# Optimization experiments

Hardware: AMD Instinct MI355X
Metric: run time of the kernel (lower is better)

## Reference

```python
import jax, jax.numpy as jnp
import numpy as np

KW = 31       # avg_pool kernel
PAD = 15      # padding (count_include_pad=True => divide by KW*KW always)


def _box_avg(x):
    # F.avg_pool2d(x, 31, stride=1, padding=15) with count_include_pad=True
    s = jax.lax.reduce_window(
        x, 0.0, jax.lax.add,
        window_dimensions=(1, 1, KW, KW),
        window_strides=(1, 1, 1, 1),
        padding=((0, 0), (0, 0), (PAD, PAD), (PAD, PAD)))
    return s / (KW * KW)


def setup_inputs() -> dict:
    key = jax.random.key(0)
    k1, k2 = jax.random.split(key)
    B, C, H, W = 64, 1, 512, 512
    pred = jax.random.normal(k1, (B, C, H, W), dtype=jnp.float32)
    mask = jax.random.uniform(k2, (B, C, H, W), dtype=jnp.float32)
    return {"pred": pred, "mask": mask}


def reference(pred, mask):
    weit = 1.0 + 5.0 * jnp.abs(_box_avg(mask) - mask)
    # stable BCE-with-logits, elementwise
    bce = jnp.maximum(pred, 0.0) - pred * mask + jnp.log1p(jnp.exp(-jnp.abs(pred)))
    # NOTE: original passes reduce='none' which PyTorch's legacy handling maps to
    # reduction='mean' -> wbce is a global scalar; the weit normalization cancels.
    wbce = bce.mean()  # scalar, broadcast over [B, C]
    p = jax.nn.sigmoid(pred)
    inter = (p * mask * weit).sum(axis=(2, 3))          # [B, C]
    union = ((p + mask) * weit).sum(axis=(2, 3))        # [B, C]
    wiou = 1.0 - (inter + 1.0) / (union - inter + 1.0)  # [B, C]
    return (wbce + wiou).mean()
```

## Files before the change

kernel.cpp:

```cpp
#include <hip/hip_runtime.h>
#include <math.h>

#define BDIM 64
#define HDIM 512
#define WDIM 512
#define KW   31
#define PAD  15
#define INV_KK (1.0f / 961.0f)
#define TH   64
#define NPIX ((size_t)BDIM * HDIM * WDIM)

#define NACC 129

__global__ void zero_acc_kernel(double* acc) {
    int i = threadIdx.x;
    if (i < NACC) acc[i] = 0.0;
}

template<int CTRL, int RMASK>
__device__ __forceinline__ float dpp_add(float p) {
    int t = __builtin_amdgcn_update_dpp(0, __builtin_bit_cast(int, p),
                                        CTRL, RMASK, 0xf, true);
    return p + __builtin_bit_cast(float, t);
}

__device__ __forceinline__ float wave_iscan(float p) {
    p = dpp_add<0x111, 0xf>(p);
    p = dpp_add<0x112, 0xf>(p);
    p = dpp_add<0x114, 0xf>(p);
    p = dpp_add<0x118, 0xf>(p);
    p = dpp_add<0x142, 0xa>(p);
    p = dpp_add<0x143, 0xc>(p);
    return p;
}

__device__ __forceinline__ float wave_iscan30(float p) {
    p = dpp_add<0x111, 0xf>(p);
    p = dpp_add<0x112, 0xf>(p);
    p = dpp_add<0x114, 0xf>(p);
    p = dpp_add<0x118, 0xf>(p);
    p = dpp_add<0x142, 0xa>(p);
    return p;
}

__device__ __forceinline__ float wave_shr1(float p) {
    int t = __builtin_amdgcn_update_dpp(0, __builtin_bit_cast(int, p),
                                        0x138 , 0xf, 0xf, true);
    return __builtin_bit_cast(float, t);
}

__global__ __launch_bounds__(512, 2)
void fused_kernel(const float* __restrict__ pred,
                  const float* __restrict__ mask,
                  double* __restrict__ acc) {
    __shared__ float ring[32][WDIM];
    __shared__ float red[3][8];

    const int b    = blockIdx.x;
    const int y0   = blockIdx.y * TH;
    const int x    = threadIdx.x;
    const int lane = x & 63;
    const int wv   = x >> 6;
    const int s    = wv * 64;

    const float* mbase = mask + (size_t)b * HDIM * WDIM;
    const float* pbase = pred + (size_t)b * HDIM * WDIM;

    const int acol = s - 15 + lane;
    const int bcol = s + 49 + lane;
    const bool a_ok = (acol >= 0) && (acol < WDIM);
    const bool b_ok = (lane < 30) && (bcol < WDIM);

    const int tstart = y0 - PAD;
    const int tend   = y0 + TH - 1 + PAD;

    float vs = 0.f;
    float bce_acc = 0.f, inter_acc = 0.f, uni_acc = 0.f;

    auto load_halo = [&](int row, float& A, float& B) {
        A = 0.f; B = 0.f;
        if (row >= 0 && row < HDIM) {
            const float* rp = mbase + (size_t)row * WDIM;
            if (a_ok) A = rp[acol];
            if (b_ok) B = rp[bcol];
        }
    };
    auto load_emit = [&](int row, float& M, float& P) {
        M = 0.f; P = 0.f;
        if (row >= y0 + PAD && row <= tend) {
            const size_t off = (size_t)(row - PAD) * WDIM + x;
            M = mbase[off];
            P = pbase[off];
        }
    };

    auto process = [&](int t, float A, float B, float M, float P) {
        float pa = wave_iscan(A);
        float pb = wave_iscan30(B);
        const float atot = __builtin_bit_cast(float,
            __builtin_amdgcn_readlane(__builtin_bit_cast(int, pa), 63));
        const float v1 = __shfl(pa, (lane + 30) & 63);
        const float v2 = __shfl(pb, (lane + 30) & 63);
        const float Phi = (lane <= 33) ? v1 : (atot + v2);
        const float Plo = wave_shr1(pa);
        const float hs  = Phi - Plo;

        vs += hs;
        if (t - KW >= tstart) vs -= ring[(t - KW) & 31][x];
        ring[t & 31][x] = hs;

        if (t >= y0 + PAD) {
            const float box  = vs * INV_KK;
            const float weit = 1.f + 5.f * fabsf(box - M);
            const float e1   = __expf(-fabsf(P));
            const float bce  = fmaxf(P, 0.f) - P * M + __logf(1.f + e1);
            const float sp   = __builtin_amdgcn_rcpf(1.f + __expf(-P));
            bce_acc   += bce;
            inter_acc += sp * M * weit;
            uni_acc   += (sp + M) * weit;
        }
    };

    float ca[2], cb[2], cm[2], cp[2];
    load_halo(tstart,     ca[0], cb[0]);
    load_halo(tstart + 1, ca[1], cb[1]);
    load_emit(tstart,     cm[0], cp[0]);
    load_emit(tstart + 1, cm[1], cp[1]);

    for (int t = tstart; t <= tend; t += 2) {
        float na[2], nb[2], nm[2], nq[2];
        load_halo(t + 2, na[0], nb[0]);
        load_halo(t + 3, na[1], nb[1]);
        load_emit(t + 2, nm[0], nq[0]);
        load_emit(t + 3, nm[1], nq[1]);

        process(t,     ca[0], cb[0], cm[0], cp[0]);
        process(t + 1, ca[1], cb[1], cm[1], cp[1]);

        ca[0] = na[0]; ca[1] = na[1]; cb[0] = nb[0]; cb[1] = nb[1];
        cm[0] = nm[0]; cm[1] = nm[1]; cp[0] = nq[0]; cp[1] = nq[1];
    }

#pragma unroll
    for (int off = 32; off > 0; off >>= 1) {
        bce_acc   += __shfl_down(bce_acc, off);
        inter_acc += __shfl_down(inter_acc, off);
        uni_acc   += __shfl_down(uni_acc, off);
    }
    if (lane == 0) {
        red[0][wv] = bce_acc;
        red[1][wv] = inter_acc;
        red[2][wv] = uni_acc;
    }
    __syncthreads();
    if (threadIdx.x == 0) {
        float bs = 0.f, is = 0.f, us = 0.f;
#pragma unroll
        for (int w = 0; w < 8; ++w) { bs += red[0][w]; is += red[1][w]; us += red[2][w]; }
        atomicAdd(&acc[0],      (double)bs);
        atomicAdd(&acc[1 + b],  (double)is);
        atomicAdd(&acc[65 + b], (double)us);
    }
}

__global__ void finalize_kernel(const double* __restrict__ acc, float* __restrict__ out) {
    const int b = threadIdx.x;
    double inter = acc[1 + b];
    double uni   = acc[65 + b];
    double wiou  = 1.0 - (inter + 1.0) / (uni - inter + 1.0);
#pragma unroll
    for (int off = 32; off > 0; off >>= 1) wiou += __shfl_down(wiou, off);
    if (b == 0) {
        double wbce = acc[0] / (double)NPIX;
        out[0] = (float)(wbce + wiou / (double)BDIM);
    }
}

extern "C" void kernel_launch(void* const* d_in, const int* in_sizes, int n_in,
                              void* d_out, int out_size, void* d_ws, size_t ws_size,
                              hipStream_t stream) {
    const float* pred = (const float*)d_in[0];
    const float* mask = (const float*)d_in[1];
    float* out = (float*)d_out;
    double* acc = (double*)d_ws;

    zero_acc_kernel<<<1, 256, 0, stream>>>(acc);

    dim3 grid(BDIM, HDIM / TH);
    fused_kernel<<<grid, WDIM, 0, stream>>>(pred, mask, acc);

    finalize_kernel<<<1, 64, 0, stream>>>(acc, out);
}
```

Before: 175.9 us.

## Move vertical sliding-window ring from LDS to registers and split blocks by width

```diff
diff --git a/kernel.cpp b/kernel.cpp
--- a/kernel.cpp
+++ b/kernel.cpp
@@ -49,19 +49,18 @@
     return __builtin_bit_cast(float, t);
 }
 
-__global__ __launch_bounds__(512, 2)
+__global__ __launch_bounds__(256, 5)
 void fused_kernel(const float* __restrict__ pred,
                   const float* __restrict__ mask,
                   double* __restrict__ acc) {
-    __shared__ float ring[32][WDIM];
-    __shared__ float red[3][8];
+    __shared__ float red[3][4];
 
     const int b    = blockIdx.x;
     const int y0   = blockIdx.y * TH;
-    const int x    = threadIdx.x;
-    const int lane = x & 63;
-    const int wv   = x >> 6;
-    const int s    = wv * 64;
+    const int x    = blockIdx.z * 256 + threadIdx.x;
+    const int lane = threadIdx.x & 63;
+    const int wv   = threadIdx.x >> 6;
+    const int s    = blockIdx.z * 256 + wv * 64;
 
     const float* mbase = mask + (size_t)b * HDIM * WDIM;
     const float* pbase = pred + (size_t)b * HDIM * WDIM;
@@ -70,75 +69,74 @@
     const int bcol = s + 49 + lane;
     const bool a_ok = (acol >= 0) && (acol < WDIM);
     const bool b_ok = (lane < 30) && (bcol < WDIM);
+    const int hi_lane = (lane + 30) & 63;
 
     const int tstart = y0 - PAD;
-    const int tend   = y0 + TH - 1 + PAD;
 
-    float vs = 0.f;
     float bce_acc = 0.f, inter_acc = 0.f, uni_acc = 0.f;
 
-    auto load_halo = [&](int row, float& A, float& B) {
-        A = 0.f; B = 0.f;
-        if (row >= 0 && row < HDIM) {
-            const float* rp = mbase + (size_t)row * WDIM;
+    auto hrow = [&](int t) -> float {
+        float A = 0.f, B = 0.f;
+        if ((unsigned)t < (unsigned)HDIM) {
+            const float* rp = mbase + (size_t)t * WDIM;
             if (a_ok) A = rp[acol];
             if (b_ok) B = rp[bcol];
         }
-    };
-    auto load_emit = [&](int row, float& M, float& P) {
-        M = 0.f; P = 0.f;
-        if (row >= y0 + PAD && row <= tend) {
-            const size_t off = (size_t)(row - PAD) * WDIM + x;
-            M = mbase[off];
-            P = pbase[off];
-        }
-    };
-
-    auto process = [&](int t, float A, float B, float M, float P) {
         float pa = wave_iscan(A);
         float pb = wave_iscan30(B);
         const float atot = __builtin_bit_cast(float,
             __builtin_amdgcn_readlane(__builtin_bit_cast(int, pa), 63));
-        const float v1 = __shfl(pa, (lane + 30) & 63);
-        const float v2 = __shfl(pb, (lane + 30) & 63);
+        const float v1 = __shfl(pa, hi_lane);
+        const float v2 = __shfl(pb, hi_lane);
         const float Phi = (lane <= 33) ? v1 : (atot + v2);
         const float Plo = wave_shr1(pa);
-        const float hs  = Phi - Plo;
-
-        vs += hs;
-        if (t - KW >= tstart) vs -= ring[(t - KW) & 31][x];
-        ring[t & 31][x] = hs;
-
-        if (t >= y0 + PAD) {
-            const float box  = vs * INV_KK;
-            const float weit = 1.f + 5.f * fabsf(box - M);
-            const float e1   = __expf(-fabsf(P));
-            const float bce  = fmaxf(P, 0.f) - P * M + __logf(1.f + e1);
-            const float sp   = __builtin_amdgcn_rcpf(1.f + __expf(-P));
-            bce_acc   += bce;
-            inter_acc += sp * M * weit;
-            uni_acc   += (sp + M) * weit;
-        }
+        return Phi - Plo;
     };
 
-    float ca[2], cb[2], cm[2], cp[2];
-    load_halo(tstart,     ca[0], cb[0]);
-    load_halo(tstart + 1, ca[1], cb[1]);
-    load_emit(tstart,     cm[0], cp[0]);
-    load_emit(tstart + 1, cm[1], cp[1]);
+    auto emit = [&](int t, float vsv) {
+        const size_t off = (size_t)(t - PAD) * WDIM + x;
+        const float M = mbase[off];
+        const float P = pbase[off];
+        const float box  = vsv * INV_KK;
+        const float weit = 1.f + 5.f * fabsf(box - M);
+        const float e1   = __expf(-fabsf(P));
+        const float bce  = fmaxf(P, 0.f) - P * M + __logf(1.f + e1);
+        const float sp   = __builtin_amdgcn_rcpf(1.f + __expf(-P));
+        bce_acc   += bce;
+        inter_acc += sp * M * weit;
+        uni_acc   += (sp + M) * weit;
+    };
 
-    for (int t = tstart; t <= tend; t += 2) {
-        float na[2], nb[2], nm[2], nq[2];
-        load_halo(t + 2, na[0], nb[0]);
-        load_halo(t + 3, na[1], nb[1]);
-        load_emit(t + 2, nm[0], nq[0]);
-        load_emit(t + 3, nm[1], nq[1]);
+    float ring[31];
+    float vs = 0.f;
 
-        process(t,     ca[0], cb[0], cm[0], cp[0]);
-        process(t + 1, ca[1], cb[1], cm[1], cp[1]);
-
-        ca[0] = na[0]; ca[1] = na[1]; cb[0] = nb[0]; cb[1] = nb[1];
-        cm[0] = nm[0]; cm[1] = nm[1]; cp[0] = nq[0]; cp[1] = nq[1];
+#pragma unroll
+    for (int r = 0; r < 30; ++r) {
+        const float h = hrow(tstart + r);
+        vs += h;
+        ring[r] = h;
+    }
+    {
+        const float h = hrow(tstart + 30);
+        vs += h;
+        ring[30] = h;
+        emit(tstart + 30, vs);
+    }
+#pragma unroll 1
+    for (int rep = 0; rep < 2; ++rep) {
+        const int t0 = tstart + 31 + rep * 31;
+#pragma unroll
+        for (int i = 0; i < 31; ++i) {
+            const float h = hrow(t0 + i);
+            vs += h - ring[i];
+            ring[i] = h;
+            emit(t0 + i, vs);
+        }
+    }
+    {
+        const float h = hrow(tstart + 93);
+        vs += h - ring[0];
+        emit(tstart + 93, vs);
     }
 
 #pragma unroll
@@ -156,7 +154,7 @@
     if (threadIdx.x == 0) {
         float bs = 0.f, is = 0.f, us = 0.f;
 #pragma unroll
-        for (int w = 0; w < 8; ++w) { bs += red[0][w]; is += red[1][w]; us += red[2][w]; }
+        for (int w = 0; w < 4; ++w) { bs += red[0][w]; is += red[1][w]; us += red[2][w]; }
         atomicAdd(&acc[0],      (double)bs);
         atomicAdd(&acc[1 + b],  (double)is);
         atomicAdd(&acc[65 + b], (double)us);
@@ -186,8 +184,8 @@
 
     zero_acc_kernel<<<1, 256, 0, stream>>>(acc);
 
-    dim3 grid(BDIM, HDIM / TH);
-    fused_kernel<<<grid, WDIM, 0, stream>>>(pred, mask, acc);
+    dim3 grid(BDIM, HDIM / TH, WDIM / 256);
+    fused_kernel<<<grid, 256, 0, stream>>>(pred, mask, acc);
 
     finalize_kernel<<<1, 64, 0, stream>>>(acc, out);
 }
```

Result: slower. 287.2 us (+63.3%).

## Split columns into bands, taller row tiles, deeper prefetch, cheaper sigmoid

Applied to the files above, without the earlier changes.

```diff
diff --git a/kernel.cpp b/kernel.cpp
--- a/kernel.cpp
+++ b/kernel.cpp
@@ -7,7 +7,8 @@
 #define KW   31
 #define PAD  15
 #define INV_KK (1.0f / 961.0f)
-#define TH   64
+#define TH   128
+#define BAND 256
 #define NPIX ((size_t)BDIM * HDIM * WDIM)
 
 #define NACC 129
@@ -49,19 +50,20 @@
     return __builtin_bit_cast(float, t);
 }
 
-__global__ __launch_bounds__(512, 2)
+__global__ __launch_bounds__(256, 2)
 void fused_kernel(const float* __restrict__ pred,
                   const float* __restrict__ mask,
                   double* __restrict__ acc) {
-    __shared__ float ring[32][WDIM];
-    __shared__ float red[3][8];
+    __shared__ float ring[32][BAND];
+    __shared__ float red[3][4];
 
     const int b    = blockIdx.x;
     const int y0   = blockIdx.y * TH;
-    const int x    = threadIdx.x;
-    const int lane = x & 63;
-    const int wv   = x >> 6;
-    const int s    = wv * 64;
+    const int tid  = threadIdx.x;
+    const int lane = tid & 63;
+    const int wv   = tid >> 6;
+    const int x    = blockIdx.z * BAND + tid;
+    const int s    = blockIdx.z * BAND + wv * 64;
 
     const float* mbase = mask + (size_t)b * HDIM * WDIM;
     const float* pbase = pred + (size_t)b * HDIM * WDIM;
@@ -70,6 +72,7 @@
     const int bcol = s + 49 + lane;
     const bool a_ok = (acol >= 0) && (acol < WDIM);
     const bool b_ok = (lane < 30) && (bcol < WDIM);
+    const int hi_lane = (lane + 30) & 63;
 
     const int tstart = y0 - PAD;
     const int tend   = y0 + TH - 1 + PAD;
@@ -77,68 +80,75 @@
     float vs = 0.f;
     float bce_acc = 0.f, inter_acc = 0.f, uni_acc = 0.f;
 
-    auto load_halo = [&](int row, float& A, float& B) {
+    auto load_halo = [&](int t, float& A, float& B) {
         A = 0.f; B = 0.f;
-        if (row >= 0 && row < HDIM) {
-            const float* rp = mbase + (size_t)row * WDIM;
+        if ((unsigned)t < (unsigned)HDIM) {
+            const float* rp = mbase + (size_t)t * WDIM;
             if (a_ok) A = rp[acol];
             if (b_ok) B = rp[bcol];
         }
     };
-    auto load_emit = [&](int row, float& M, float& P) {
+    auto load_emit = [&](int t, float& M, float& P) {
         M = 0.f; P = 0.f;
-        if (row >= y0 + PAD && row <= tend) {
-            const size_t off = (size_t)(row - PAD) * WDIM + x;
+        if (t >= y0 + PAD && t <= tend) {
+            const size_t off = (size_t)(t - PAD) * WDIM + x;
             M = mbase[off];
             P = pbase[off];
         }
     };
 
-    auto process = [&](int t, float A, float B, float M, float P) {
+    auto process = [&](int t, float A, float B, float M, float P, float rr) {
         float pa = wave_iscan(A);
         float pb = wave_iscan30(B);
         const float atot = __builtin_bit_cast(float,
             __builtin_amdgcn_readlane(__builtin_bit_cast(int, pa), 63));
-        const float v1 = __shfl(pa, (lane + 30) & 63);
-        const float v2 = __shfl(pb, (lane + 30) & 63);
+        const float v1 = __shfl(pa, hi_lane);
+        const float v2 = __shfl(pb, hi_lane);
         const float Phi = (lane <= 33) ? v1 : (atot + v2);
         const float Plo = wave_shr1(pa);
         const float hs  = Phi - Plo;
 
-        vs += hs;
-        if (t - KW >= tstart) vs -= ring[(t - KW) & 31][x];
-        ring[t & 31][x] = hs;
+        vs += hs - rr;
+        ring[t & 31][tid] = hs;
 
         if (t >= y0 + PAD) {
             const float box  = vs * INV_KK;
             const float weit = 1.f + 5.f * fabsf(box - M);
             const float e1   = __expf(-fabsf(P));
+            const float den  = __builtin_amdgcn_rcpf(1.f + e1);
+            const float sp   = ((P >= 0.f) ? 1.f : e1) * den;
             const float bce  = fmaxf(P, 0.f) - P * M + __logf(1.f + e1);
-            const float sp   = __builtin_amdgcn_rcpf(1.f + __expf(-P));
             bce_acc   += bce;
             inter_acc += sp * M * weit;
             uni_acc   += (sp + M) * weit;
         }
     };
 
-    float ca[2], cb[2], cm[2], cp[2];
-    load_halo(tstart,     ca[0], cb[0]);
-    load_halo(tstart + 1, ca[1], cb[1]);
-    load_emit(tstart,     cm[0], cp[0]);
-    load_emit(tstart + 1, cm[1], cp[1]);
+    float cA0,cB0,cM0,cP0, cA1,cB1,cM1,cP1;
+    float nA0,nB0,nM0,nP0, nA1,nB1,nM1,nP1;
+    load_halo(tstart,     cA0, cB0); load_emit(tstart,     cM0, cP0);
+    load_halo(tstart + 1, cA1, cB1); load_emit(tstart + 1, cM1, cP1);
+    load_halo(tstart + 2, nA0, nB0); load_emit(tstart + 2, nM0, nP0);
+    load_halo(tstart + 3, nA1, nB1); load_emit(tstart + 3, nM1, nP1);
+    float rr0 = 0.f, rr1 = 0.f;
 
     for (int t = tstart; t <= tend; t += 2) {
-        float na[2], nb[2], nm[2], nq[2];
-        load_halo(t + 2, na[0], nb[0]);
-        load_halo(t + 3, na[1], nb[1]);
-        load_emit(t + 2, nm[0], nq[0]);
-        load_emit(t + 3, nm[1], nq[1]);
-
-        process(t,     ca[0], cb[0], cm[0], cp[0]);
-        process(t + 1, ca[1], cb[1], cm[1], cp[1]);
-
-        ca[0] = na[0]; ca[1] = na[1]; cb[0] = nb[0]; cb[1] = nb[1];
-        cm[0] = nm[0]; cm[1] = nm[1]; cp[0] = nq[0]; cp[1] = nq[1];
+        float fA0=0.f,fB0=0.f,fM0=0.f,fP0=0.f, fA1=0.f,fB1=0.f,fM1=0.f,fP1=0.f;
+        if (t + 4 <= tend) { load_halo(t + 4, fA0, fB0); load_emit(t + 4, fM0, fP0); }
+        if (t + 5 <= tend) { load_halo(t + 5, fA1, fB1); load_emit(t + 5, fM1, fP1); }
+
+        float pr0 = 0.f, pr1 = 0.f;
+        if (t + 2 - KW >= tstart) pr0 = ring[(t + 2 - KW) & 31][tid];
+        if (t + 3 - KW >= tstart) pr1 = ring[(t + 3 - KW) & 31][tid];
+
+        process(t,     cA0, cB0, cM0, cP0, rr0);
+        process(t + 1, cA1, cB1, cM1, cP1, rr1);
+
+        cA0=nA0; cB0=nB0; cM0=nM0; cP0=nP0;
+        cA1=nA1; cB1=nB1; cM1=nM1; cP1=nP1;
+        nA0=fA0; nB0=fB0; nM0=fM0; nP0=fP0;
+        nA1=fA1; nB1=fB1; nM1=fM1; nP1=fP1;
+        rr0=pr0; rr1=pr1;
     }
 
 #pragma unroll
@@ -156,7 +166,7 @@
     if (threadIdx.x == 0) {
         float bs = 0.f, is = 0.f, us = 0.f;
 #pragma unroll
-        for (int w = 0; w < 8; ++w) { bs += red[0][w]; is += red[1][w]; us += red[2][w]; }
+        for (int w = 0; w < 4; ++w) { bs += red[0][w]; is += red[1][w]; us += red[2][w]; }
         atomicAdd(&acc[0],      (double)bs);
         atomicAdd(&acc[1 + b],  (double)is);
         atomicAdd(&acc[65 + b], (double)us);
@@ -186,8 +196,8 @@
 
     zero_acc_kernel<<<1, 256, 0, stream>>>(acc);
 
-    dim3 grid(BDIM, HDIM / TH);
-    fused_kernel<<<grid, WDIM, 0, stream>>>(pred, mask, acc);
+    dim3 grid(BDIM, HDIM / TH, WDIM / BAND);
+    fused_kernel<<<grid, 256, 0, stream>>>(pred, mask, acc);
 
     finalize_kernel<<<1, 64, 0, stream>>>(acc, out);
 }
```

Result: slower. 179.6 us (+2.1%).
